# Performance work log

Hardware: AMD Instinct MI355X
Metric: run time of the kernel (lower is better)

The kernel has to match this reference:

```python
import jax, jax.numpy as jnp
import numpy as np

N = 50000      # nodes
E = 800000     # edges (before self-loops)
F_IN = 128     # num_node_features
H = 4          # heads
C = 32         # graph_hidden_channels (per head)
HC = H * C     # 128
NHID = 512
NOUT = 768
G = 256        # graphs in batch
NEG_SLOPE = 0.2


def setup_inputs() -> dict:
    key = jax.random.key(0)
    ks = jax.random.split(key, 32)
    s = 0.05
    inp = {
        "x": jax.random.normal(ks[0], (N, F_IN), jnp.float32),
        "edge_index": jax.random.randint(ks[1], (2, E), 0, N, jnp.int64),
        "batch": jnp.sort(jax.random.randint(ks[2], (N,), 0, G, jnp.int64)),
    }
    dims = [F_IN, HC, HC]
    k = 3
    for i, din in enumerate(dims, start=1):
        inp[f"w{i}"] = jax.random.normal(ks[k], (din, HC), jnp.float32) * s; k += 1
        inp[f"as{i}"] = jax.random.normal(ks[k], (H, C), jnp.float32) * s; k += 1
        inp[f"ad{i}"] = jax.random.normal(ks[k], (H, C), jnp.float32) * s; k += 1
        inp[f"b{i}"] = jnp.zeros((HC,), jnp.float32)
        inp[f"sk{i}w"] = jax.random.normal(ks[k], (din, HC), jnp.float32) * s; k += 1
        inp[f"sk{i}b"] = jnp.zeros((HC,), jnp.float32)
    inp["m1w"] = jax.random.normal(ks[k], (HC, NHID), jnp.float32) * s; k += 1
    inp["m1b"] = jnp.zeros((NHID,), jnp.float32)
    inp["m2w"] = jax.random.normal(ks[k], (NHID, NOUT), jnp.float32) * s
    inp["m2b"] = jnp.zeros((NOUT,), jnp.float32)
    return inp


def _gat_conv(x, src, dst, W, a_src, a_dst, b):
    # x: [N, din]; src/dst: [E+N] (self-loops included)
    n = x.shape[0]
    h = (x @ W).reshape(n, H, C)                       # [N, H, C]
    e_src = jnp.sum(h * a_src, axis=-1)                # [N, H]
    e_dst = jnp.sum(h * a_dst, axis=-1)                # [N, H]
    e = jax.nn.leaky_relu(e_src[src] + e_dst[dst], NEG_SLOPE)  # [E', H]
    m = jax.ops.segment_max(e, dst, num_segments=n)    # segment softmax (stable)
    ex = jnp.exp(e - m[dst])
    z = jax.ops.segment_sum(ex, dst, num_segments=n)
    alpha = ex / z[dst]                                # [E', H]
    out = jax.ops.segment_sum(alpha[:, :, None] * h[src], dst, num_segments=n)
    return out.reshape(n, HC) + b


def reference(x, edge_index, batch,
              w1, as1, ad1, b1, sk1w, sk1b,
              w2, as2, ad2, b2, sk2w, sk2b,
              w3, as3, ad3, b3, sk3w, sk3b,
              m1w, m1b, m2w, m2b):
    n = x.shape[0]
    loops = jnp.arange(n, dtype=edge_index.dtype)
    src = jnp.concatenate([edge_index[0], loops])      # PyG add_self_loops=True
    dst = jnp.concatenate([edge_index[1], loops])

    h = jax.nn.relu(x @ sk1w + sk1b + _gat_conv(x, src, dst, w1, as1, ad1, b1))
    h = jax.nn.relu(h @ sk2w + sk2b + _gat_conv(h, src, dst, w2, as2, ad2, b2))
    h = jax.nn.relu(h @ sk3w + sk3b + _gat_conv(h, src, dst, w3, as3, ad3, b3))

    pooled = jax.ops.segment_max(h, batch, num_segments=G)  # global_max_pool
    pooled = jnp.where(jnp.isfinite(pooled), pooled, 0.0)   # guard empty graphs
    out = jax.nn.relu(pooled @ m1w + m1b)
    out = out @ m2w + m2b
    return out
```

## Files before the change

### kernel.cpp

```cpp
#include <hip/hip_runtime.h>
#include <hip/hip_bf16.h>
#include <math.h>

#define NN 50000
#define EE 800000
#define EPE 850000
#define HCC 128
#define GGR 256
#define NHIDD 512
#define NOUTD 768
#define CHUNK 256
#define CPAD (CHUNK + 8)
#define SCAN_NBLK ((NN + 1023) / 1024)
#define MBLK ((NN + 63) / 64)

typedef __attribute__((ext_vector_type(8))) short bf16x8;
typedef __attribute__((ext_vector_type(4))) float f32x4;

__device__ __forceinline__ void atomicMaxF(float* addr, float v) {
    if (v >= 0.f) atomicMax(reinterpret_cast<int*>(addr), __float_as_int(v));
    else atomicMin(reinterpret_cast<unsigned int*>(addr), __float_as_uint(v));
}

__device__ __forceinline__ float lrelu(float x) { return x > 0.f ? x : 0.2f * x; }

__device__ __forceinline__ ushort f2bf(float f) {
    unsigned u = __float_as_uint(f);
    unsigned r = (u + 0x7fffu + ((u >> 16) & 1u)) >> 16;
    return (ushort)r;
}
__device__ __forceinline__ float bf2f(ushort b) {
    return __uint_as_float(((unsigned)b) << 16);
}

__global__ void conv_x(const float* __restrict__ X, ushort* __restrict__ Xb) {
    int i = blockIdx.x * 256 + threadIdx.x;
    if (i < NN * HCC / 4) {
        float4 v = reinterpret_cast<const float4*>(X)[i];
        ushort4 o;
        o.x = f2bf(v.x); o.y = f2bf(v.y); o.z = f2bf(v.z); o.w = f2bf(v.w);
        reinterpret_cast<ushort4*>(Xb)[i] = o;
    }
}

__global__ void conv_w(const float* __restrict__ W, const float* __restrict__ SKW,
                       ushort* __restrict__ Wt) {
    int i = blockIdx.x * 256 + threadIdx.x;
    if (i >= 256 * 128) return;
    int n = i >> 7, k = i & 127;
    float v = (n < 128) ? W[(size_t)k * 128 + n] : SKW[(size_t)k * 128 + (n - 128)];
    Wt[i] = f2bf(v);
}

__global__ void hist_zero(int* __restrict__ counts) {
    int i = blockIdx.x * 256 + threadIdx.x;
    if (i < NN) counts[i] = 0;
}

__global__ void hist(const int* __restrict__ ei, int* __restrict__ counts) {
    int e = blockIdx.x * 256 + threadIdx.x;
    if (e >= EPE) return;
    int d = (e < EE) ? ei[EE + e] : e - EE;
    atomicAdd(&counts[d], 1);
}

__global__ __launch_bounds__(256) void scan_partial(const int* __restrict__ counts,
                                                    int* __restrict__ excl,
                                                    int* __restrict__ blocksums)
{
    __shared__ int s[256];
    const int b = blockIdx.x, t = threadIdx.x;
    const int idx = b * 1024 + t * 4;
    int a0 = (idx + 0 < NN) ? counts[idx + 0] : 0;
    int a1 = (idx + 1 < NN) ? counts[idx + 1] : 0;
    int a2 = (idx + 2 < NN) ? counts[idx + 2] : 0;
    int a3 = (idx + 3 < NN) ? counts[idx + 3] : 0;
    int sum4 = a0 + a1 + a2 + a3;
    s[t] = sum4;
    __syncthreads();
    #pragma unroll
    for (int off = 1; off < 256; off <<= 1) {
        int add = (t >= off) ? s[t - off] : 0;
        __syncthreads();
        s[t] += add;
        __syncthreads();
    }
    int e0 = s[t] - sum4;
    if (idx + 0 < NN) excl[idx + 0] = e0;
    if (idx + 1 < NN) excl[idx + 1] = e0 + a0;
    if (idx + 2 < NN) excl[idx + 2] = e0 + a0 + a1;
    if (idx + 3 < NN) excl[idx + 3] = e0 + a0 + a1 + a2;
    if (t == 255) blocksums[b] = s[255];
}

__global__ __launch_bounds__(64) void scan_sums(int* __restrict__ blocksums,
                                                int* __restrict__ blockoffs,
                                                int* __restrict__ row_start)
{
    __shared__ int s[64];
    int t = threadIdx.x;
    int v = (t < SCAN_NBLK) ? blocksums[t] : 0;
    s[t] = v;
    __syncthreads();
    #pragma unroll
    for (int off = 1; off < 64; off <<= 1) {
        int add = (t >= off) ? s[t - off] : 0;
        __syncthreads();
        s[t] += add;
        __syncthreads();
    }
    if (t < SCAN_NBLK) blockoffs[t] = s[t] - v;
    if (t == 63) row_start[NN] = s[63];
}

__global__ void scan_add(const int* __restrict__ excl, const int* __restrict__ blockoffs,
                         int* __restrict__ row_start, int* __restrict__ cursor)
{
    int i = blockIdx.x * 256 + threadIdx.x;
    if (i >= NN) return;
    int v = excl[i] + blockoffs[i >> 10];
    row_start[i] = v;
    cursor[i] = v;
}

__global__ void scatter_csr(const int* __restrict__ ei, int* __restrict__ cursor,
                            int* __restrict__ csr_src) {
    int e = blockIdx.x * 256 + threadIdx.x;
    if (e >= EPE) return;
    int s, d;
    if (e < EE) { s = ei[e]; d = ei[EE + e]; } else { s = d = e - EE; }
    int pos = atomicAdd(&cursor[d], 1);
    csr_src[pos] = s;
}

__global__ __launch_bounds__(256) void gemm_mfma(
    const ushort* __restrict__ Xb,
    const ushort* __restrict__ Wt,
    const float* __restrict__ skb, const float* __restrict__ bb,
    ushort* __restrict__ Hout, float* __restrict__ Agg)
{
    __shared__ ushort Xs[64 * 128];
    const int r0 = blockIdx.x * 64;
    const int tid = threadIdx.x;
    const int w = tid >> 6;
    const int l = tid & 63;
    const int lm = l & 15;
    const int lk = l >> 4;

    #pragma unroll
    for (int it = 0; it < 4; ++it) {
        int slot = it * 256 + tid;
        int row = slot >> 4;
        int bc = (slot & 15) << 4;
        int n = r0 + row;
        bf16x8 v = (bf16x8)(short)0;
        if (n < NN) v = *reinterpret_cast<const bf16x8*>(Xb + (size_t)n * 128 + (bc >> 1));
        *reinterpret_cast<bf16x8*>(reinterpret_cast<char*>(Xs) + row * 256 + (bc ^ ((row & 7) << 4))) = v;
    }
    __syncthreads();

    f32x4 acc[4][4];
    #pragma unroll
    for (int nb = 0; nb < 4; ++nb)
        #pragma unroll
        for (int rf = 0; rf < 4; ++rf)
            acc[nb][rf] = (f32x4){0.f, 0.f, 0.f, 0.f};

    #pragma unroll
    for (int ks = 0; ks < 4; ++ks) {
        bf16x8 a[4];
        #pragma unroll
        for (int rf = 0; rf < 4; ++rf) {
            int row = rf * 16 + lm;
            int bc = (ks * 32 + lk * 8) * 2;
            a[rf] = *reinterpret_cast<const bf16x8*>(
                reinterpret_cast<const char*>(Xs) + row * 256 + (bc ^ ((row & 7) << 4)));
        }
        #pragma unroll
        for (int nb = 0; nb < 4; ++nb) {
            int ncol = (w * 4 + nb) * 16 + lm;
            bf16x8 b = *reinterpret_cast<const bf16x8*>(Wt + (size_t)ncol * 128 + ks * 32 + lk * 8);
            #pragma unroll
            for (int rf = 0; rf < 4; ++rf)
                acc[nb][rf] = __builtin_amdgcn_mfma_f32_16x16x32_bf16(a[rf], b, acc[nb][rf], 0, 0, 0);
        }
    }

    #pragma unroll
    for (int nb = 0; nb < 4; ++nb) {
        int ncol = (w * 4 + nb) * 16 + lm;
        #pragma unroll
        for (int rf = 0; rf < 4; ++rf) {
            #pragma unroll
            for (int r = 0; r < 4; ++r) {
                int n = r0 + rf * 16 + lk * 4 + r;
                if (n >= NN) continue;
                float v = acc[nb][rf][r];
                if (ncol < 128) {
                    Hout[(size_t)n * 128 + ncol] = f2bf(v);
                } else {
                    int c = ncol - 128;
                    Agg[(size_t)n * 128 + c] = v + skb[c] + bb[c];
                }
            }
        }
    }
}

__global__ __launch_bounds__(256) void node_attn(
    const ushort* __restrict__ Hb, const float* __restrict__ as_, const float* __restrict__ ad_,
    float* __restrict__ esrc, float* __restrict__ edst)
{
    int tid = threadIdx.x;
    int node = blockIdx.x * 2 + (tid >> 7);
    int t = tid & 127;
    if (node >= NN) return;
    float hv = bf2f(Hb[(size_t)node * 128 + t]);
    float p1 = hv * as_[t];
    float p2 = hv * ad_[t];
    #pragma unroll
    for (int o = 16; o > 0; o >>= 1) {
        p1 += __shfl_down(p1, o, 32);
        p2 += __shfl_down(p2, o, 32);
    }
    if ((t & 31) == 0) {
        esrc[node * 4 + (t >> 5)] = p1;
        edst[node * 4 + (t >> 5)] = p2;
    }
}

__global__ __launch_bounds__(128) void gat_aggr(
    const int* __restrict__ row_start, const int* __restrict__ csr_src,
    const float* __restrict__ esrc, const float* __restrict__ edst,
    const ushort* __restrict__ Hb, const float* __restrict__ skipagg,
    ushort* __restrict__ outbuf)
{
    __shared__ int   lsrc[CHUNK];
    __shared__ float lw[4][CPAD];
    __shared__ float shsc[4];
    __shared__ float accbuf[8][HCC];
    const int d = blockIdx.x;
    const int t = threadIdx.x;
    const int hd = t >> 5;
    const int l = t & 31;
    const int slot = t >> 4;
    const int cg = t & 15;
    const int c0 = cg * 8;
    const int ghd = cg >> 2;
    const int r0 = row_start[d], r1 = row_start[d + 1];
    const float4 edv = *reinterpret_cast<const float4*>(edst + (size_t)d * 4);
    float acc[8] = {0.f, 0.f, 0.f, 0.f, 0.f, 0.f, 0.f, 0.f};
    float m_h = -INFINITY, z_h = 0.f;

    for (int base = r0; base < r1; base += CHUNK) {
        const int nc = min(CHUNK, r1 - base);
        __syncthreads();
        for (int i = t; i < nc; i += 128) {
            int s = csr_src[base + i];
            lsrc[i] = s;
            float4 ev = *reinterpret_cast<const float4*>(esrc + (size_t)s * 4);
            lw[0][i] = lrelu(ev.x + edv.x);
            lw[1][i] = lrelu(ev.y + edv.y);
            lw[2][i] = lrelu(ev.z + edv.z);
            lw[3][i] = lrelu(ev.w + edv.w);
        }
        __syncthreads();
        float mx = m_h;
        for (int i = l; i < nc; i += 32) mx = fmaxf(mx, lw[hd][i]);
        #pragma unroll
        for (int off = 16; off > 0; off >>= 1) mx = fmaxf(mx, __shfl_xor(mx, off, 32));
        float sc = __expf(m_h - mx);
        float zp = 0.f;
        for (int i = l; i < nc; i += 32) {
            float w = __expf(lw[hd][i] - mx);
            lw[hd][i] = w;
            zp += w;
        }
        #pragma unroll
        for (int off = 16; off > 0; off >>= 1) zp += __shfl_xor(zp, off, 32);
        z_h = z_h * sc + zp;
        m_h = mx;
        if (l == 0) shsc[hd] = sc;
        __syncthreads();
        float scg = shsc[ghd];
        #pragma unroll
        for (int j = 0; j < 8; ++j) acc[j] *= scg;
        for (int i = slot; i < nc; i += 8) {
            int s = lsrc[i];
            float wgt = lw[ghd][i];
            bf16x8 row = *reinterpret_cast<const bf16x8*>(Hb + (size_t)s * 128 + c0);
            #pragma unroll
            for (int j = 0; j < 8; ++j)
                acc[j] = fmaf(wgt, bf2f((ushort)row[j]), acc[j]);
        }
    }
    #pragma unroll
    for (int j = 0; j < 8; ++j) accbuf[slot][c0 + j] = acc[j];
    __syncthreads();
    float tot = 0.f;
    #pragma unroll
    for (int s = 0; s < 8; ++s) tot += accbuf[s][t];
    float res = skipagg[(size_t)d * 128 + t] + tot / z_h;
    outbuf[(size_t)d * 128 + t] = f2bf(fmaxf(res, 0.f));
}

__global__ void pool_init(float* __restrict__ pooled) {
    int i = blockIdx.x * 256 + threadIdx.x;
    if (i < GGR * HCC) pooled[i] = -INFINITY;
}

__global__ void pool_max(const ushort* __restrict__ xf, const int* __restrict__ batch,
                         float* __restrict__ pooled)
{
    int i = blockIdx.x * 256 + threadIdx.x;
    if (i >= NN * HCC) return;
    int n = i >> 7, c = i & 127;
    atomicMaxF(&pooled[batch[n] * 128 + c], bf2f(xf[i]));
}

__global__ __launch_bounds__(512) void mlp1(const float* __restrict__ pooled,
                                            const float* __restrict__ w,
                                            const float* __restrict__ bias,
                                            float* __restrict__ hid)
{
    __shared__ float xs[128];
    int g = blockIdx.x, t = threadIdx.x;
    if (t < 128) {
        float v = pooled[g * 128 + t];
        if (!isfinite(v)) v = 0.f;
        xs[t] = v;
    }
    __syncthreads();
    float acc = 0.f;
    #pragma unroll 8
    for (int k = 0; k < 128; ++k) acc += xs[k] * w[(size_t)k * NHIDD + t];
    hid[(size_t)g * NHIDD + t] = fmaxf(acc + bias[t], 0.f);
}

__global__ __launch_bounds__(768) void mlp2(const float* __restrict__ hid,
                                            const float* __restrict__ w,
                                            const float* __restrict__ bias,
                                            float* __restrict__ out)
{
    __shared__ float xs[NHIDD];
    int g = blockIdx.x, t = threadIdx.x;
    if (t < NHIDD) xs[t] = hid[(size_t)g * NHIDD + t];
    __syncthreads();
    float acc = 0.f;
    #pragma unroll 8
    for (int k = 0; k < NHIDD; ++k) acc += xs[k] * w[(size_t)k * NOUTD + t];
    out[(size_t)g * NOUTD + t] = acc + bias[t];
}

extern "C" void kernel_launch(void* const* d_in, const int* in_sizes, int n_in,
                              void* d_out, int out_size, void* d_ws, size_t ws_size,
                              hipStream_t stream)
{
    const float* x = (const float*)d_in[0];
    const int* ei = (const int*)d_in[1];
    const int* batch = (const int*)d_in[2];
    const float* W[3]   = {(const float*)d_in[3],  (const float*)d_in[9],  (const float*)d_in[15]};
    const float* AS[3]  = {(const float*)d_in[4],  (const float*)d_in[10], (const float*)d_in[16]};
    const float* AD[3]  = {(const float*)d_in[5],  (const float*)d_in[11], (const float*)d_in[17]};
    const float* B[3]   = {(const float*)d_in[6],  (const float*)d_in[12], (const float*)d_in[18]};
    const float* SKW[3] = {(const float*)d_in[7],  (const float*)d_in[13], (const float*)d_in[19]};
    const float* SKB[3] = {(const float*)d_in[8],  (const float*)d_in[14], (const float*)d_in[20]};
    const float* m1w = (const float*)d_in[21];
    const float* m1b = (const float*)d_in[22];
    const float* m2w = (const float*)d_in[23];
    const float* m2b = (const float*)d_in[24];
    float* out = (float*)d_out;

    float* p = (float*)d_ws;
    ushort* bufA = (ushort*)p; p += (size_t)NN * HCC / 2;
    ushort* bufB = (ushort*)p; p += (size_t)NN * HCC / 2;
    ushort* xb   = (ushort*)p; p += (size_t)NN * HCC / 2;
    ushort* hbuf = (ushort*)p; p += (size_t)NN * HCC / 2;
    ushort* wt3  = (ushort*)p; p += 3 * 256 * 128 / 2;
    float* agg  = p; p += (size_t)NN * HCC;
    float* esrc = p; p += NN * 4;
    float* edst = p; p += NN * 4;
    float* pooled = p; p += GGR * HCC;
    float* hidden = p; p += GGR * NHIDD;
    int* counts    = (int*)p; p += NN;
    int* excl      = (int*)p; p += NN;
    int* row_start = (int*)p; p += NN + 4;
    int* cursor    = (int*)p; p += NN;
    int* csr_src   = (int*)p; p += EPE;
    int* blocksums = (int*)p; p += 64;
    int* blockoffs = (int*)p; p += 64;

    conv_x<<<(NN * HCC / 4 + 255) / 256, 256, 0, stream>>>(x, xb);
    for (int l = 0; l < 3; ++l)
        conv_w<<<(256 * 128 + 255) / 256, 256, 0, stream>>>(W[l], SKW[l], wt3 + l * 256 * 128);

    hist_zero<<<(NN + 255) / 256, 256, 0, stream>>>(counts);
    hist<<<(EPE + 255) / 256, 256, 0, stream>>>(ei, counts);
    scan_partial<<<SCAN_NBLK, 256, 0, stream>>>(counts, excl, blocksums);
    scan_sums<<<1, 64, 0, stream>>>(blocksums, blockoffs, row_start);
    scan_add<<<(NN + 255) / 256, 256, 0, stream>>>(excl, blockoffs, row_start, cursor);
    scatter_csr<<<(EPE + 255) / 256, 256, 0, stream>>>(ei, cursor, csr_src);

    const ushort* cur = xb;
    ushort* outs[3] = {bufA, bufB, bufA};
    for (int l = 0; l < 3; ++l) {
        gemm_mfma<<<MBLK, 256, 0, stream>>>(cur, wt3 + l * 256 * 128, SKB[l], B[l], hbuf, agg);
        node_attn<<<NN / 2, 256, 0, stream>>>(hbuf, AS[l], AD[l], esrc, edst);
        gat_aggr<<<NN, 128, 0, stream>>>(row_start, csr_src, esrc, edst, hbuf, agg, outs[l]);
        cur = outs[l];
    }
    pool_init<<<(GGR * HCC) / 256, 256, 0, stream>>>(pooled);
    pool_max<<<(NN * HCC + 255) / 256, 256, 0, stream>>>(cur, batch, pooled);
    mlp1<<<GGR, NHIDD, 0, stream>>>(pooled, m1w, m1b, hidden);
    mlp2<<<GGR, NOUTD, 0, stream>>>(hidden, m2w, m2b, out);
}
```

Measured before the change: 545.3 us.

## Replicate CSR histogram/cursors 8x and pool via sorted-batch run reduction

The degree histogram and scatter cursors are split into 8 replicas selected by block index, so atomics on the same destination node are spread across copies. The scan sums the replicas and assigns each one a sub-range of the row. Global max pooling now uses the sorted batch array: each thread reduces a run of 16 nodes locally and issues one atomic per graph change instead of one per element. The cost is extra zeroing and memory traffic for the 8 replica arrays, and the CSR order within a row now differs.

```diff
diff --git a/kernel.cpp b/kernel.cpp
--- a/kernel.cpp
+++ b/kernel.cpp
@@ -13,6 +13,8 @@
 #define CPAD (CHUNK + 8)
 #define SCAN_NBLK ((NN + 1023) / 1024)
 #define MBLK ((NN + 63) / 64)
+#define NPAD 50176
+#define NREP 8
 
 typedef __attribute__((ext_vector_type(8))) short bf16x8;
 typedef __attribute__((ext_vector_type(4))) float f32x4;
@@ -52,30 +54,37 @@
     Wt[i] = f2bf(v);
 }
 
-__global__ void hist_zero(int* __restrict__ counts) {
+__global__ void hist_zero8(int* __restrict__ cnt8) {
     int i = blockIdx.x * 256 + threadIdx.x;
-    if (i < NN) counts[i] = 0;
-}
-
-__global__ void hist(const int* __restrict__ ei, int* __restrict__ counts) {
+    if (i < NREP * NPAD) cnt8[i] = 0;
+}
+
+__global__ void hist8(const int* __restrict__ ei, int* __restrict__ cnt8) {
     int e = blockIdx.x * 256 + threadIdx.x;
     if (e >= EPE) return;
+    int rep = blockIdx.x & 7;
     int d = (e < EE) ? ei[EE + e] : e - EE;
-    atomicAdd(&counts[d], 1);
-}
-
-__global__ __launch_bounds__(256) void scan_partial(const int* __restrict__ counts,
+    atomicAdd(&cnt8[rep * NPAD + d], 1);
+}
+
+__global__ __launch_bounds__(256) void scan_partial(const int* __restrict__ cnt8,
                                                     int* __restrict__ excl,
                                                     int* __restrict__ blocksums)
 {
     __shared__ int s[256];
     const int b = blockIdx.x, t = threadIdx.x;
     const int idx = b * 1024 + t * 4;
-    int a0 = (idx + 0 < NN) ? counts[idx + 0] : 0;
-    int a1 = (idx + 1 < NN) ? counts[idx + 1] : 0;
-    int a2 = (idx + 2 < NN) ? counts[idx + 2] : 0;
-    int a3 = (idx + 3 < NN) ? counts[idx + 3] : 0;
-    int sum4 = a0 + a1 + a2 + a3;
+    int a[4] = {0, 0, 0, 0};
+    #pragma unroll
+    for (int j = 0; j < 4; ++j) {
+        if (idx + j < NN) {
+            int tot = 0;
+            #pragma unroll
+            for (int r = 0; r < NREP; ++r) tot += cnt8[r * NPAD + idx + j];
+            a[j] = tot;
+        }
+    }
+    int sum4 = a[0] + a[1] + a[2] + a[3];
     s[t] = sum4;
     __syncthreads();
     #pragma unroll
@@ -87,9 +96,9 @@
     }
     int e0 = s[t] - sum4;
     if (idx + 0 < NN) excl[idx + 0] = e0;
-    if (idx + 1 < NN) excl[idx + 1] = e0 + a0;
-    if (idx + 2 < NN) excl[idx + 2] = e0 + a0 + a1;
-    if (idx + 3 < NN) excl[idx + 3] = e0 + a0 + a1 + a2;
+    if (idx + 1 < NN) excl[idx + 1] = e0 + a[0];
+    if (idx + 2 < NN) excl[idx + 2] = e0 + a[0] + a[1];
+    if (idx + 3 < NN) excl[idx + 3] = e0 + a[0] + a[1] + a[2];
     if (t == 255) blocksums[b] = s[255];
 }
 
@@ -114,22 +123,29 @@
 }
 
 __global__ void scan_add(const int* __restrict__ excl, const int* __restrict__ blockoffs,
-                         int* __restrict__ row_start, int* __restrict__ cursor)
+                         const int* __restrict__ cnt8,
+                         int* __restrict__ row_start, int* __restrict__ cur8)
 {
     int i = blockIdx.x * 256 + threadIdx.x;
     if (i >= NN) return;
     int v = excl[i] + blockoffs[i >> 10];
     row_start[i] = v;
-    cursor[i] = v;
-}
-
-__global__ void scatter_csr(const int* __restrict__ ei, int* __restrict__ cursor,
-                            int* __restrict__ csr_src) {
+    int c = v;
+    #pragma unroll
+    for (int r = 0; r < NREP; ++r) {
+        cur8[r * NPAD + i] = c;
+        c += cnt8[r * NPAD + i];
+    }
+}
+
+__global__ void scatter_csr8(const int* __restrict__ ei, int* __restrict__ cur8,
+                             int* __restrict__ csr_src) {
     int e = blockIdx.x * 256 + threadIdx.x;
     if (e >= EPE) return;
+    int rep = blockIdx.x & 7;
     int s, d;
     if (e < EE) { s = ei[e]; d = ei[EE + e]; } else { s = d = e - EE; }
-    int pos = atomicAdd(&cursor[d], 1);
+    int pos = atomicAdd(&cur8[rep * NPAD + d], 1);
     csr_src[pos] = s;
 }
 
@@ -309,13 +325,33 @@
     if (i < GGR * HCC) pooled[i] = -INFINITY;
 }
 
-__global__ void pool_max(const ushort* __restrict__ xf, const int* __restrict__ batch,
-                         float* __restrict__ pooled)
-{
-    int i = blockIdx.x * 256 + threadIdx.x;
-    if (i >= NN * HCC) return;
-    int n = i >> 7, c = i & 127;
-    atomicMaxF(&pooled[batch[n] * 128 + c], bf2f(xf[i]));
+__global__ __launch_bounds__(256) void pool_max_sorted(
+    const ushort* __restrict__ xf, const int* __restrict__ batch,
+    float* __restrict__ pooled)
+{
+    __shared__ int gb[32];
+    const int n0 = blockIdx.x * 32;
+    const int t = threadIdx.x;
+    if (t < 32) gb[t] = (n0 + t < NN) ? batch[n0 + t] : -1;
+    __syncthreads();
+    const int c = t & 127;
+    const int half = t >> 7;
+    int curg = -1;
+    float curv = -INFINITY;
+    #pragma unroll 4
+    for (int i = 0; i < 16; ++i) {
+        int n = n0 + half * 16 + i;
+        if (n >= NN) break;
+        int g = gb[half * 16 + i];
+        float v = bf2f(xf[(size_t)n * 128 + c]);
+        if (g != curg) {
+            if (curg >= 0) atomicMaxF(&pooled[curg * 128 + c], curv);
+            curg = g; curv = v;
+        } else {
+            curv = fmaxf(curv, v);
+        }
+    }
+    if (curg >= 0) atomicMaxF(&pooled[curg * 128 + c], curv);
 }
 
 __global__ __launch_bounds__(512) void mlp1(const float* __restrict__ pooled,
@@ -382,10 +418,10 @@
     float* edst = p; p += NN * 4;
     float* pooled = p; p += GGR * HCC;
     float* hidden = p; p += GGR * NHIDD;
-    int* counts    = (int*)p; p += NN;
+    int* cnt8      = (int*)p; p += NREP * NPAD;
+    int* cur8      = (int*)p; p += NREP * NPAD;
     int* excl      = (int*)p; p += NN;
     int* row_start = (int*)p; p += NN + 4;
-    int* cursor    = (int*)p; p += NN;
     int* csr_src   = (int*)p; p += EPE;
     int* blocksums = (int*)p; p += 64;
     int* blockoffs = (int*)p; p += 64;
@@ -394,12 +430,12 @@
     for (int l = 0; l < 3; ++l)
         conv_w<<<(256 * 128 + 255) / 256, 256, 0, stream>>>(W[l], SKW[l], wt3 + l * 256 * 128);
 
-    hist_zero<<<(NN + 255) / 256, 256, 0, stream>>>(counts);
-    hist<<<(EPE + 255) / 256, 256, 0, stream>>>(ei, counts);
-    scan_partial<<<SCAN_NBLK, 256, 0, stream>>>(counts, excl, blocksums);
+    hist_zero8<<<(NREP * NPAD + 255) / 256, 256, 0, stream>>>(cnt8);
+    hist8<<<(EPE + 255) / 256, 256, 0, stream>>>(ei, cnt8);
+    scan_partial<<<SCAN_NBLK, 256, 0, stream>>>(cnt8, excl, blocksums);
     scan_sums<<<1, 64, 0, stream>>>(blocksums, blockoffs, row_start);
-    scan_add<<<(NN + 255) / 256, 256, 0, stream>>>(excl, blockoffs, row_start, cursor);
-    scatter_csr<<<(EPE + 255) / 256, 256, 0, stream>>>(ei, cursor, csr_src);
+    scan_add<<<(NN + 255) / 256, 256, 0, stream>>>(excl, blockoffs, cnt8, row_start, cur8);
+    scatter_csr8<<<(EPE + 255) / 256, 256, 0, stream>>>(ei, cur8, csr_src);
 
     const ushort* cur = xb;
     ushort* outs[3] = {bufA, bufB, bufA};
@@ -410,7 +446,7 @@
         cur = outs[l];
     }
     pool_init<<<(GGR * HCC) / 256, 256, 0, stream>>>(pooled);
-    pool_max<<<(NN * HCC + 255) / 256, 256, 0, stream>>>(cur, batch, pooled);
+    pool_max_sorted<<<(NN + 31) / 32, 256, 0, stream>>>(cur, batch, pooled);
     mlp1<<<GGR, NHIDD, 0, stream>>>(pooled, m1w, m1b, hidden);
     mlp2<<<GGR, NOUTD, 0, stream>>>(hidden, m2w, m2b, out);
 }
```

Result: faster. 528.0 us (-3.2%).
